# Kernel optimization log

Hardware: AMD Instinct MI355X
Metric: run time of the kernel (lower is better)

## Reference

```python
import jax, jax.numpy as jnp
import numpy as np

H = 128
M = 50000
L = 400000
EPS = 1e-9


def setup_inputs() -> dict:
    key = jax.random.key(0)
    ks = jax.random.split(key, 24)
    d = {
        'x_emb': jax.random.normal(ks[0], (M, H), jnp.float32),
        'child_h': jax.random.normal(ks[1], (M, H), jnp.float32),
        'child_c': jax.random.normal(ks[2], (M, H), jnp.float32),
        'pair_cand_idx': jax.random.randint(ks[3], (L,), 0, M, jnp.int32),
        'pair_child_idx': jax.random.randint(ks[4], (L,), 0, M, jnp.int32),
    }
    s = 1.0 / np.sqrt(H)
    names = ['Wi_w', 'Ui_w', 'Wf_w', 'Uf_w', 'Wo_w', 'Uo_w', 'Wc_w', 'Uc_w', 'Wa_w', 'Ua_w']
    for i, n in enumerate(names):
        d[n] = jax.random.uniform(ks[5 + i], (H, H), jnp.float32, -s, s)
    for i, n in enumerate(['Wi_b', 'Wf_b', 'Wo_b', 'Wc_b', 'Wa_b']):
        d[n] = jax.random.uniform(ks[15 + i], (H,), jnp.float32, -s, s)
    d['v_w'] = jax.random.uniform(ks[20], (H,), jnp.float32, -s, s)
    return d


def reference(x_emb, child_h, child_c, pair_cand_idx, pair_child_idx,
              Wi_w, Ui_w, Wf_w, Uf_w, Wo_w, Uo_w, Wc_w, Uc_w, Wa_w, Ua_w,
              Wi_b, Wf_b, Wo_b, Wc_b, Wa_b, v_w):
    m = x_emb.shape[0]
    ci, chi = pair_cand_idx, pair_child_idx

    # --- segment attention (torch version runs under no_grad) ---
    Ah = child_h @ Wa_w.T + Wa_b          # [M,H]
    Bx = x_emb @ Ua_w.T                   # [M,H]
    e = jnp.tanh(Ah[chi] + Bx[ci]) @ v_w  # [L]
    seg_max = jax.ops.segment_max(e, ci, num_segments=m)
    x_exp = jnp.exp(e - seg_max[ci])
    seg_sum = jax.ops.segment_sum(x_exp, ci, num_segments=m) + EPS
    attn = x_exp / seg_sum[ci]            # [L]
    h_hat = jax.ops.segment_sum(attn[:, None] * child_h[chi], ci, num_segments=m)  # [M,H]

    # --- tree-LSTM gates ---
    i_j = jax.nn.sigmoid(x_emb @ Wi_w.T + Wi_b + h_hat @ Ui_w.T)
    Wfx = x_emb @ Wf_w.T + Wf_b
    Ufh = child_h @ Uf_w.T
    f_pair = jax.nn.sigmoid(Wfx[ci] + Ufh[chi])                       # [L,H]
    sum_f_c = jax.ops.segment_sum(f_pair * child_c[chi], ci, num_segments=m)
    c_t = jnp.tanh(x_emb @ Wc_w.T + Wc_b + h_hat @ Uc_w.T)
    c = i_j * c_t + sum_f_c
    o_j = jax.nn.sigmoid(x_emb @ Wo_w.T + Wo_b + h_hat @ Uo_w.T)
    h = o_j * jnp.tanh(c)
    return (h, c)
```

## Files before the change

kernel.cpp:

```cpp
#include <hip/hip_runtime.h>
#include <cstdint>
#include <cstddef>

#define H 128
#define PSTRIDE 512

typedef __bf16 v8bf __attribute__((ext_vector_type(8)));
typedef __bf16 v4bf __attribute__((ext_vector_type(4)));
typedef float  v4f  __attribute__((ext_vector_type(4)));

__device__ __forceinline__ float ftanh(float x) {
    return 1.f - 2.f / (1.f + __expf(2.f * x));
}
__device__ __forceinline__ float fsigm(float x) {
    return 1.f / (1.f + __expf(-x));
}

struct Stage { const __bf16* W; const float* bias; __bf16* C; int ldc; };
struct MultiDesc { const void* A; int lda; int af32; int ns; Stage st[5]; };
struct MultiBatch { MultiDesc g[2]; };
struct WPtrs { const float* w[10]; };

__global__ __launch_bounds__(256) void prep_k(WPtrs wp, __bf16* __restrict__ Wb,
                                              const float* __restrict__ chh,
                                              const float* __restrict__ chc,
                                              __bf16* __restrict__ P,
                                              const int* __restrict__ ci,
                                              int* __restrict__ counts,
                                              int MH4, int L) {
    int tid = blockIdx.x * 256 + threadIdx.x;
    if (tid < 40960) {
        int mat = tid >> 12;
        int off = (tid & 4095) << 2;
        v4f a = *(const v4f*)(wp.w[mat] + off);
        v4bf b;
#pragma unroll
        for (int k = 0; k < 4; ++k) b[k] = (__bf16)a[k];
        *(v4bf*)(Wb + mat * 16384 + off) = b;
        return;
    }
    int i = tid - 40960;
    if (i < MH4) {
        v4f b = ((const v4f*)chh)[i];
        v4f c = ((const v4f*)chc)[i];
        v4bf bb, cb;
#pragma unroll
        for (int k = 0; k < 4; ++k) { bb[k] = (__bf16)b[k]; cb[k] = (__bf16)c[k]; }
        int m = i >> 5;
        int q = (i & 31) << 2;
        __bf16* prow = P + (size_t)m * PSTRIDE + q;
        *(v4bf*)prow = bb;
        *(v4bf*)(prow + H) = cb;
        return;
    }
    int l = i - MH4;
    if (l < L) atomicAdd(&counts[ci[l]], 1);
}

__global__ __launch_bounds__(256) void gemm_multi(MultiBatch mb, int M) {
    const MultiDesc d = mb.g[blockIdx.y];
    __shared__ __bf16 wlds[H][H + 8];

    const int wave = threadIdx.x >> 6;
    const int lane = threadIdx.x & 63;
    const int quad = lane >> 4;
    const int l16  = lane & 15;
    const int r0   = blockIdx.x * 128 + wave * 32;

    int ra = r0 + l16;      if (ra > M - 1) ra = M - 1;
    int rb = r0 + 16 + l16; if (rb > M - 1) rb = M - 1;

    v8bf a0[4], a1[4];
    if (d.af32) {
        const float* A = (const float*)d.A;
        const float* p0 = A + (size_t)ra * d.lda + quad * 8;
        const float* p1 = A + (size_t)rb * d.lda + quad * 8;
#pragma unroll
        for (int k0 = 0; k0 < 4; ++k0) {
            v4f x0a = *(const v4f*)(p0 + k0 * 32);
            v4f x0b = *(const v4f*)(p0 + k0 * 32 + 4);
            v4f x1a = *(const v4f*)(p1 + k0 * 32);
            v4f x1b = *(const v4f*)(p1 + k0 * 32 + 4);
            v8bf t0, t1;
#pragma unroll
            for (int k = 0; k < 4; ++k) {
                t0[k] = (__bf16)x0a[k]; t0[k + 4] = (__bf16)x0b[k];
                t1[k] = (__bf16)x1a[k]; t1[k + 4] = (__bf16)x1b[k];
            }
            a0[k0] = t0; a1[k0] = t1;
        }
    } else {
        const __bf16* A = (const __bf16*)d.A;
        const __bf16* p0 = A + (size_t)ra * d.lda + quad * 8;
        const __bf16* p1 = A + (size_t)rb * d.lda + quad * 8;
#pragma unroll
        for (int k0 = 0; k0 < 4; ++k0) {
            a0[k0] = *(const v8bf*)(p0 + k0 * 32);
            a1[k0] = *(const v8bf*)(p1 + k0 * 32);
        }
    }

    for (int s = 0; s < d.ns; ++s) {
        if (s) __syncthreads();
        for (int t = threadIdx.x; t < 2048; t += 256) {
            int n = t >> 4;
            int k = (t & 15) << 3;
            *(v8bf*)&wlds[n][k] = *(const v8bf*)(d.st[s].W + n * H + k);
        }
        __syncthreads();

        v4f acc0[8], acc1[8];
#pragma unroll
        for (int nt = 0; nt < 8; ++nt) {
            acc0[nt] = (v4f){0.f, 0.f, 0.f, 0.f};
            acc1[nt] = (v4f){0.f, 0.f, 0.f, 0.f};
        }
#pragma unroll
        for (int k0 = 0; k0 < 4; ++k0) {
#pragma unroll
            for (int nt = 0; nt < 8; ++nt) {
                v8bf b = *(const v8bf*)(&wlds[nt * 16 + l16][k0 * 32 + quad * 8]);
                acc0[nt] = __builtin_amdgcn_mfma_f32_16x16x32_bf16(a0[k0], b, acc0[nt], 0, 0, 0);
                acc1[nt] = __builtin_amdgcn_mfma_f32_16x16x32_bf16(a1[k0], b, acc1[nt], 0, 0, 0);
            }
        }

        const float* bias = d.st[s].bias;
        __bf16* C = d.st[s].C;
        const int ldc = d.st[s].ldc;
#pragma unroll
        for (int nt = 0; nt < 8; ++nt) {
            int n = nt * 16 + l16;
            float bia = bias ? bias[n] : 0.f;
#pragma unroll
            for (int r = 0; r < 4; ++r) {
                int m0 = r0 + quad * 4 + r;
                int m1 = m0 + 16;
                if (m0 < M) C[(size_t)m0 * ldc + n] = (__bf16)(acc0[nt][r] + bia);
                if (m1 < M) C[(size_t)m1 * ldc + n] = (__bf16)(acc1[nt][r] + bia);
            }
        }
    }
}

__global__ __launch_bounds__(256) void edge_score(const int* __restrict__ ci,
                                                  const int* __restrict__ chi,
                                                  const float* __restrict__ vw,
                                                  const __bf16* __restrict__ Bx,
                                                  const __bf16* __restrict__ P,
                                                  float* __restrict__ ex_out, int L) {
    int e = blockIdx.x * 8 + (threadIdx.x >> 5);
    if (e >= L) return;
    const int l32 = threadIdx.x & 31;
    const int h = l32 << 2;
    int m  = ci[e];
    int cj = chi[e];

    v4bf a4 = *(const v4bf*)(P + (cj << 9) + 3 * H + h);
    v4bf b4 = *(const v4bf*)(Bx + (m << 7) + h);
    v4f  vv = *(const v4f*)(vw + h);

    float s = 0.f;
#pragma unroll
    for (int k = 0; k < 4; ++k) s += ftanh((float)a4[k] + (float)b4[k]) * vv[k];
    s += __shfl_xor(s, 1);
    s += __shfl_xor(s, 2);
    s += __shfl_xor(s, 4);
    s += __shfl_xor(s, 8);
    s += __shfl_xor(s, 16);
    if (l32 == 0) ex_out[e] = __expf(s);
}

__global__ __launch_bounds__(1024) void scan_local(const int* __restrict__ counts,
                                                   int* __restrict__ excl,
                                                   int* __restrict__ bsums, int M) {
    __shared__ int s[1024];
    int tid = threadIdx.x;
    int idx = blockIdx.x * 1024 + tid;
    int v = (idx < M) ? counts[idx] : 0;
    s[tid] = v;
    __syncthreads();
    for (int off = 1; off < 1024; off <<= 1) {
        int t = (tid >= off) ? s[tid - off] : 0;
        __syncthreads();
        s[tid] += t;
        __syncthreads();
    }
    if (idx < M) excl[idx] = s[tid] - v;
    if (tid == 1023) bsums[blockIdx.x] = s[1023];
}

__global__ __launch_bounds__(1024) void scan_fused(int* __restrict__ rowptr,
                                                   int* __restrict__ cursor,
                                                   const int* __restrict__ bsums,
                                                   const int* __restrict__ counts,
                                                   int M, int nb) {
    __shared__ int s[1024];
    int t = threadIdx.x, b = blockIdx.x;
    int v = (t < nb) ? bsums[t] : 0;
    s[t] = v;
    __syncthreads();
    for (int off = 1; off < 1024; off <<= 1) {
        int tt = (t >= off) ? s[t - off] : 0;
        __syncthreads();
        s[t] += tt;
        __syncthreads();
    }
    int boff = (b == 0) ? 0 : s[b - 1];
    int idx = b * 1024 + t;
    if (idx < M) {
        int val = rowptr[idx] + boff;
        rowptr[idx] = val;
        cursor[idx] = val;
        if (idx == M - 1) rowptr[M] = val + counts[M - 1];
    }
}

__global__ __launch_bounds__(256) void scatter_k(const int* __restrict__ ci,
                                                 const int* __restrict__ chi,
                                                 const float* __restrict__ ex_e,
                                                 int* __restrict__ cursor,
                                                 int* __restrict__ payload,
                                                 float* __restrict__ exs, int L) {
    int l = blockIdx.x * 256 + threadIdx.x;
    if (l < L) {
        float ex = ex_e[l];
        int c = chi[l];
        int pos = atomicAdd(&cursor[ci[l]], 1);
        payload[pos] = c;
        exs[pos] = ex;
    }
}

__global__ __launch_bounds__(256) void segment_fused(const int* __restrict__ rowptr,
                                                     const int* __restrict__ payload,
                                                     const float* __restrict__ exs,
                                                     const __bf16* __restrict__ Wfx,
                                                     const __bf16* __restrict__ P,
                                                     __bf16* __restrict__ hhat,
                                                     float* __restrict__ sumfc, int M) {
    const int wl   = threadIdx.x & 63;
    const int half = wl & 32;
    const int l32  = wl & 31;
    const int m = blockIdx.x * 8 + (threadIdx.x >> 5);
    if (m >= M) return;
    const int start = rowptr[m];
    const int deg   = rowptr[m + 1] - start;
    const int h = l32 << 2;

    v4bf wf4 = *(const v4bf*)(Wfx + (m << 7) + h);
    float wff[4];
#pragma unroll
    for (int k = 0; k < 4; ++k) wff[k] = (float)wf4[k];

    int   pl0 = (l32 < deg) ? payload[start + l32] : 0;
    int   pl1 = (32 + l32 < deg) ? payload[start + 32 + l32] : 0;
    float ex0 = (l32 < deg) ? exs[start + l32] : 0.f;
    float ex1 = (32 + l32 < deg) ? exs[start + 32 + l32] : 0.f;

    float denom = 0.f;
    float acch[4] = {0.f, 0.f, 0.f, 0.f};
    float accf[4] = {0.f, 0.f, 0.f, 0.f};

    const int jcap = deg < 64 ? deg : 64;
    for (int j = 0; j < jcap; ++j) {
        int   cj = __shfl((j & 32) ? pl1 : pl0, half | (j & 31), 64);
        float ex = __shfl((j & 32) ? ex1 : ex0, half | (j & 31), 64);
        int off = (cj << 9) + h;
        v4bf h4 = *(const v4bf*)(P + off);
        v4bf c4 = *(const v4bf*)(P + off + H);
        v4bf u4 = *(const v4bf*)(P + off + 2 * H);
        denom += ex;
#pragma unroll
        for (int k = 0; k < 4; ++k) {
            acch[k] = fmaf(ex, (float)h4[k], acch[k]);
            accf[k] += fsigm(wff[k] + (float)u4[k]) * (float)c4[k];
        }
    }
    for (int j = 64; j < deg; ++j) {
        int   cj = payload[start + j];
        float ex = exs[start + j];
        int off = (cj << 9) + h;
        v4bf h4 = *(const v4bf*)(P + off);
        v4bf c4 = *(const v4bf*)(P + off + H);
        v4bf u4 = *(const v4bf*)(P + off + 2 * H);
        denom += ex;
#pragma unroll
        for (int k = 0; k < 4; ++k) {
            acch[k] = fmaf(ex, (float)h4[k], acch[k]);
            accf[k] += fsigm(wff[k] + (float)u4[k]) * (float)c4[k];
        }
    }

    float inv = 1.f / (denom + 1e-9f);
    v4bf hb;
    v4f sf;
#pragma unroll
    for (int k = 0; k < 4; ++k) { hb[k] = (__bf16)(acch[k] * inv); sf[k] = accf[k]; }
    *(v4bf*)(hhat + (size_t)m * H + h) = hb;
    *(v4f*)(sumfc + (size_t)m * H + h) = sf;
}

__global__ __launch_bounds__(256) void gemm_final(const __bf16* __restrict__ hhat,
                                                  const __bf16* __restrict__ Ui,
                                                  const __bf16* __restrict__ Uc,
                                                  const __bf16* __restrict__ Uo,
                                                  const __bf16* __restrict__ Xi,
                                                  const __bf16* __restrict__ Xc,
                                                  const __bf16* __restrict__ Xo,
                                                  const float* __restrict__ sumfc,
                                                  float* __restrict__ out, int M, int MH) {
    __shared__ __bf16 wl[3][H][H + 8];

    for (int t = threadIdx.x; t < 6144; t += 256) {
        int w = t >> 11;
        int n = (t >> 4) & 127;
        int k = (t & 15) << 3;
        const __bf16* src = (w == 0) ? Ui : (w == 1) ? Uc : Uo;
        *(v8bf*)&wl[w][n][k] = *(const v8bf*)(src + n * H + k);
    }
    __syncthreads();

    const int wave = threadIdx.x >> 6;
    const int lane = threadIdx.x & 63;
    const int quad = lane >> 4;
    const int l16  = lane & 15;
    const int r0   = blockIdx.x * 128 + wave * 32;

    const __bf16* p0 = hhat + (size_t)(r0 + l16) * H + quad * 8;
    const __bf16* p1 = hhat + (size_t)(r0 + 16 + l16) * H + quad * 8;
    v8bf a0[4], a1[4];
#pragma unroll
    for (int k0 = 0; k0 < 4; ++k0) {
        a0[k0] = *(const v8bf*)(p0 + k0 * 32);
        a1[k0] = *(const v8bf*)(p1 + k0 * 32);
    }

#pragma unroll
    for (int nt = 0; nt < 8; ++nt) {
        v4f ai0 = (v4f){0.f, 0.f, 0.f, 0.f}, ai1 = ai0;
        v4f ac0 = ai0, ac1 = ai0, ao0 = ai0, ao1 = ai0;
#pragma unroll
        for (int k0 = 0; k0 < 4; ++k0) {
            v8bf bi = *(const v8bf*)(&wl[0][nt * 16 + l16][k0 * 32 + quad * 8]);
            v8bf bc = *(const v8bf*)(&wl[1][nt * 16 + l16][k0 * 32 + quad * 8]);
            v8bf bo = *(const v8bf*)(&wl[2][nt * 16 + l16][k0 * 32 + quad * 8]);
            ai0 = __builtin_amdgcn_mfma_f32_16x16x32_bf16(a0[k0], bi, ai0, 0, 0, 0);
            ai1 = __builtin_amdgcn_mfma_f32_16x16x32_bf16(a1[k0], bi, ai1, 0, 0, 0);
            ac0 = __builtin_amdgcn_mfma_f32_16x16x32_bf16(a0[k0], bc, ac0, 0, 0, 0);
            ac1 = __builtin_amdgcn_mfma_f32_16x16x32_bf16(a1[k0], bc, ac1, 0, 0, 0);
            ao0 = __builtin_amdgcn_mfma_f32_16x16x32_bf16(a0[k0], bo, ao0, 0, 0, 0);
            ao1 = __builtin_amdgcn_mfma_f32_16x16x32_bf16(a1[k0], bo, ao1, 0, 0, 0);
        }
        int n = nt * 16 + l16;
#pragma unroll
        for (int r = 0; r < 4; ++r) {
            int m0 = r0 + quad * 4 + r;
            if (m0 < M) {
                size_t idx = (size_t)m0 * H + n;
                float ig = fsigm((float)Xi[idx] + ai0[r]);
                float ct = ftanh((float)Xc[idx] + ac0[r]);
                float og = fsigm((float)Xo[idx] + ao0[r]);
                float c = ig * ct + sumfc[idx];
                out[idx] = og * ftanh(c);
                out[MH + idx] = c;
            }
            int m1 = m0 + 16;
            if (m1 < M) {
                size_t idx = (size_t)m1 * H + n;
                float ig = fsigm((float)Xi[idx] + ai1[r]);
                float ct = ftanh((float)Xc[idx] + ac1[r]);
                float og = fsigm((float)Xo[idx] + ao1[r]);
                float c = ig * ct + sumfc[idx];
                out[idx] = og * ftanh(c);
                out[MH + idx] = c;
            }
        }
    }
}

extern "C" void kernel_launch(void* const* d_in, const int* in_sizes, int n_in,
                              void* d_out, int out_size, void* d_ws, size_t ws_size,
                              hipStream_t stream) {
    const float* x_emb   = (const float*)d_in[0];
    const float* child_h = (const float*)d_in[1];
    const float* child_c = (const float*)d_in[2];
    const int*   ci      = (const int*)d_in[3];
    const int*   chi     = (const int*)d_in[4];
    const float* Wi_b = (const float*)d_in[15];
    const float* Wf_b = (const float*)d_in[16];
    const float* Wo_b = (const float*)d_in[17];
    const float* Wc_b = (const float*)d_in[18];
    const float* Wa_b = (const float*)d_in[19];
    const float* vw   = (const float*)d_in[20];

    const int M    = in_sizes[0] / H;
    const int L    = in_sizes[3];
    const int Mpad = (M + 127) & ~127;
    const int MH   = M * H;
    const int MH4  = MH / 4;

    char* p = (char*)d_ws;
    auto alloc = [&](size_t bytes) {
        char* r = p;
        p += (bytes + 255) & ~(size_t)255;
        return (void*)r;
    };
    size_t bfbytes = (size_t)Mpad * H * sizeof(__bf16);
    __bf16* P      = (__bf16*)alloc((size_t)Mpad * PSTRIDE * sizeof(__bf16));
    __bf16* hhat16 = (__bf16*)alloc(bfbytes);
    __bf16* Bx16   = (__bf16*)alloc(bfbytes);
    __bf16* Wfx16  = (__bf16*)alloc(bfbytes);
    __bf16* Xi16   = (__bf16*)alloc(bfbytes);
    __bf16* Xc16   = (__bf16*)alloc(bfbytes);
    __bf16* Xo16   = (__bf16*)alloc(bfbytes);
    __bf16* Wb     = (__bf16*)alloc(10 * 16384 * sizeof(__bf16));
    float* sumfc   = (float*)alloc((size_t)MH * 4);
    float* ex_e    = (float*)alloc((size_t)L * 4);
    float* exs     = (float*)alloc((size_t)L * 4);
    int*   payload = (int*)alloc((size_t)L * 4);
    int*   counts  = (int*)alloc((size_t)M * 4);
    int*   rowptr  = (int*)alloc((size_t)(M + 1) * 4);
    int*   cursor  = (int*)alloc((size_t)M * 4);
    int*   bsums   = (int*)alloc(1024 * 4);

    hipMemsetAsync(counts, 0, (size_t)M * 4, stream);

    WPtrs wp;
    for (int k = 0; k < 10; ++k) wp.w[k] = (const float*)d_in[5 + k];
    int prep_items = 40960 + MH4 + L;
    prep_k<<<(prep_items + 255) / 256, 256, 0, stream>>>(wp, Wb, child_h, child_c,
                                                         P, ci, counts, MH4, L);

    const __bf16* Wi = Wb + 0 * 16384;
    const __bf16* Ui = Wb + 1 * 16384;
    const __bf16* Wf = Wb + 2 * 16384;
    const __bf16* Uf = Wb + 3 * 16384;
    const __bf16* Wo = Wb + 4 * 16384;
    const __bf16* Uo = Wb + 5 * 16384;
    const __bf16* Wc = Wb + 6 * 16384;
    const __bf16* Uc = Wb + 7 * 16384;
    const __bf16* Wa = Wb + 8 * 16384;
    const __bf16* Ua = Wb + 9 * 16384;

    MultiBatch mb{};
    mb.g[0].A = x_emb; mb.g[0].lda = H; mb.g[0].af32 = 1; mb.g[0].ns = 5;
    mb.g[0].st[0] = Stage{Ua, nullptr, Bx16, H};
    mb.g[0].st[1] = Stage{Wf, Wf_b, Wfx16, H};
    mb.g[0].st[2] = Stage{Wi, Wi_b, Xi16, H};
    mb.g[0].st[3] = Stage{Wc, Wc_b, Xc16, H};
    mb.g[0].st[4] = Stage{Wo, Wo_b, Xo16, H};
    mb.g[1].A = P; mb.g[1].lda = PSTRIDE; mb.g[1].af32 = 0; mb.g[1].ns = 2;
    mb.g[1].st[0] = Stage{Wa, Wa_b, P + 3 * H, PSTRIDE};
    mb.g[1].st[1] = Stage{Uf, nullptr, P + 2 * H, PSTRIDE};
    gemm_multi<<<dim3(Mpad / 128, 2), 256, 0, stream>>>(mb, M);

    edge_score<<<(L + 7) / 8, 256, 0, stream>>>(ci, chi, vw, Bx16, P, ex_e, L);

    int nb = (M + 1023) / 1024;
    scan_local<<<nb, 1024, 0, stream>>>(counts, rowptr, bsums, M);
    scan_fused<<<nb, 1024, 0, stream>>>(rowptr, cursor, bsums, counts, M, nb);

    scatter_k<<<(L + 255) / 256, 256, 0, stream>>>(ci, chi, ex_e, cursor, payload, exs, L);

    segment_fused<<<(M + 7) / 8, 256, 0, stream>>>(rowptr, payload, exs, Wfx16, P,
                                                   hhat16, sumfc, M);

    gemm_final<<<Mpad / 128, 256, 0, stream>>>(hhat16, Ui, Uc, Uo, Xi16, Xc16, Xo16,
                                               sumfc, (float*)d_out, M, MH);
}
```

Before: 479.5 us.

## Split multi-stage GEMM into one block per weight, pre-convert x_emb to bf16

```diff
diff --git a/kernel.cpp b/kernel.cpp
--- a/kernel.cpp
+++ b/kernel.cpp
@@ -16,14 +16,22 @@
     return 1.f / (1.f + __expf(-x));
 }
 
-struct Stage { const __bf16* W; const float* bias; __bf16* C; int ldc; };
-struct MultiDesc { const void* A; int lda; int af32; int ns; Stage st[5]; };
-struct MultiBatch { MultiDesc g[2]; };
+struct MatDesc {
+    const __bf16* A;
+    int           lda;
+    const __bf16* Wb;
+    const float*  bias;
+    __bf16*       C;
+    int           ldc;
+};
+struct MatBatch { MatDesc m[7]; };
 struct WPtrs { const float* w[10]; };
 
 __global__ __launch_bounds__(256) void prep_k(WPtrs wp, __bf16* __restrict__ Wb,
+                                              const float* __restrict__ x,
                                               const float* __restrict__ chh,
                                               const float* __restrict__ chc,
+                                              __bf16* __restrict__ xe,
                                               __bf16* __restrict__ P,
                                               const int* __restrict__ ci,
                                               int* __restrict__ counts,
@@ -41,11 +49,15 @@
     }
     int i = tid - 40960;
     if (i < MH4) {
+        v4f a = ((const v4f*)x)[i];
         v4f b = ((const v4f*)chh)[i];
         v4f c = ((const v4f*)chc)[i];
-        v4bf bb, cb;
-#pragma unroll
-        for (int k = 0; k < 4; ++k) { bb[k] = (__bf16)b[k]; cb[k] = (__bf16)c[k]; }
+        v4bf ab, bb, cb;
+#pragma unroll
+        for (int k = 0; k < 4; ++k) {
+            ab[k] = (__bf16)a[k]; bb[k] = (__bf16)b[k]; cb[k] = (__bf16)c[k];
+        }
+        ((v4bf*)xe)[i] = ab;
         int m = i >> 5;
         int q = (i & 31) << 2;
         __bf16* prow = P + (size_t)m * PSTRIDE + q;
@@ -57,9 +69,16 @@
     if (l < L) atomicAdd(&counts[ci[l]], 1);
 }
 
-__global__ __launch_bounds__(256) void gemm_multi(MultiBatch mb, int M) {
-    const MultiDesc d = mb.g[blockIdx.y];
+__global__ __launch_bounds__(256) void gemm_batch(MatBatch batch, int M) {
+    const MatDesc d = batch.m[blockIdx.y];
     __shared__ __bf16 wlds[H][H + 8];
+
+    for (int t = threadIdx.x; t < 2048; t += 256) {
+        int n = t >> 4;
+        int k = (t & 15) << 3;
+        *(v8bf*)&wlds[n][k] = *(const v8bf*)(d.Wb + n * H + k);
+    }
+    __syncthreads();
 
     const int wave = threadIdx.x >> 6;
     const int lane = threadIdx.x & 63;
@@ -67,78 +86,37 @@
     const int l16  = lane & 15;
     const int r0   = blockIdx.x * 128 + wave * 32;
 
-    int ra = r0 + l16;      if (ra > M - 1) ra = M - 1;
-    int rb = r0 + 16 + l16; if (rb > M - 1) rb = M - 1;
-
-    v8bf a0[4], a1[4];
-    if (d.af32) {
-        const float* A = (const float*)d.A;
-        const float* p0 = A + (size_t)ra * d.lda + quad * 8;
-        const float* p1 = A + (size_t)rb * d.lda + quad * 8;
-#pragma unroll
-        for (int k0 = 0; k0 < 4; ++k0) {
-            v4f x0a = *(const v4f*)(p0 + k0 * 32);
-            v4f x0b = *(const v4f*)(p0 + k0 * 32 + 4);
-            v4f x1a = *(const v4f*)(p1 + k0 * 32);
-            v4f x1b = *(const v4f*)(p1 + k0 * 32 + 4);
-            v8bf t0, t1;
-#pragma unroll
-            for (int k = 0; k < 4; ++k) {
-                t0[k] = (__bf16)x0a[k]; t0[k + 4] = (__bf16)x0b[k];
-                t1[k] = (__bf16)x1a[k]; t1[k + 4] = (__bf16)x1b[k];
-            }
-            a0[k0] = t0; a1[k0] = t1;
-        }
-    } else {
-        const __bf16* A = (const __bf16*)d.A;
-        const __bf16* p0 = A + (size_t)ra * d.lda + quad * 8;
-        const __bf16* p1 = A + (size_t)rb * d.lda + quad * 8;
-#pragma unroll
-        for (int k0 = 0; k0 < 4; ++k0) {
-            a0[k0] = *(const v8bf*)(p0 + k0 * 32);
-            a1[k0] = *(const v8bf*)(p1 + k0 * 32);
-        }
-    }
-
-    for (int s = 0; s < d.ns; ++s) {
-        if (s) __syncthreads();
-        for (int t = threadIdx.x; t < 2048; t += 256) {
-            int n = t >> 4;
-            int k = (t & 15) << 3;
-            *(v8bf*)&wlds[n][k] = *(const v8bf*)(d.st[s].W + n * H + k);
-        }
-        __syncthreads();
-
-        v4f acc0[8], acc1[8];
+    v4f acc0[8], acc1[8];
+#pragma unroll
+    for (int nt = 0; nt < 8; ++nt) {
+        acc0[nt] = (v4f){0.f, 0.f, 0.f, 0.f};
+        acc1[nt] = (v4f){0.f, 0.f, 0.f, 0.f};
+    }
+
+    const __bf16* ar0 = d.A + (size_t)(r0 + l16) * d.lda + quad * 8;
+    const __bf16* ar1 = d.A + (size_t)(r0 + 16 + l16) * d.lda + quad * 8;
+#pragma unroll
+    for (int k0 = 0; k0 < H; k0 += 32) {
+        v8bf a0 = *(const v8bf*)(ar0 + k0);
+        v8bf a1 = *(const v8bf*)(ar1 + k0);
 #pragma unroll
         for (int nt = 0; nt < 8; ++nt) {
-            acc0[nt] = (v4f){0.f, 0.f, 0.f, 0.f};
-            acc1[nt] = (v4f){0.f, 0.f, 0.f, 0.f};
-        }
-#pragma unroll
-        for (int k0 = 0; k0 < 4; ++k0) {
-#pragma unroll
-            for (int nt = 0; nt < 8; ++nt) {
-                v8bf b = *(const v8bf*)(&wlds[nt * 16 + l16][k0 * 32 + quad * 8]);
-                acc0[nt] = __builtin_amdgcn_mfma_f32_16x16x32_bf16(a0[k0], b, acc0[nt], 0, 0, 0);
-                acc1[nt] = __builtin_amdgcn_mfma_f32_16x16x32_bf16(a1[k0], b, acc1[nt], 0, 0, 0);
-            }
-        }
-
-        const float* bias = d.st[s].bias;
-        __bf16* C = d.st[s].C;
-        const int ldc = d.st[s].ldc;
-#pragma unroll
-        for (int nt = 0; nt < 8; ++nt) {
-            int n = nt * 16 + l16;
-            float bia = bias ? bias[n] : 0.f;
-#pragma unroll
-            for (int r = 0; r < 4; ++r) {
-                int m0 = r0 + quad * 4 + r;
-                int m1 = m0 + 16;
-                if (m0 < M) C[(size_t)m0 * ldc + n] = (__bf16)(acc0[nt][r] + bia);
-                if (m1 < M) C[(size_t)m1 * ldc + n] = (__bf16)(acc1[nt][r] + bia);
-            }
+            v8bf b = *(const v8bf*)(&wlds[nt * 16 + l16][k0 + quad * 8]);
+            acc0[nt] = __builtin_amdgcn_mfma_f32_16x16x32_bf16(a0, b, acc0[nt], 0, 0, 0);
+            acc1[nt] = __builtin_amdgcn_mfma_f32_16x16x32_bf16(a1, b, acc1[nt], 0, 0, 0);
+        }
+    }
+
+#pragma unroll
+    for (int nt = 0; nt < 8; ++nt) {
+        int n = nt * 16 + l16;
+        float bia = d.bias ? d.bias[n] : 0.f;
+#pragma unroll
+        for (int r = 0; r < 4; ++r) {
+            int m0 = r0 + quad * 4 + r;
+            int m1 = m0 + 16;
+            if (m0 < M) d.C[(size_t)m0 * d.ldc + n] = (__bf16)(acc0[nt][r] + bia);
+            if (m1 < M) d.C[(size_t)m1 * d.ldc + n] = (__bf16)(acc1[nt][r] + bia);
         }
     }
 }
@@ -301,7 +279,7 @@
     *(v4f*)(sumfc + (size_t)m * H + h) = sf;
 }
 
-__global__ __launch_bounds__(256) void gemm_final(const __bf16* __restrict__ hhat,
+__global__ __launch_bounds__(512) void gemm_final(const __bf16* __restrict__ hhat,
                                                   const __bf16* __restrict__ Ui,
                                                   const __bf16* __restrict__ Uc,
                                                   const __bf16* __restrict__ Uo,
@@ -312,7 +290,7 @@
                                                   float* __restrict__ out, int M, int MH) {
     __shared__ __bf16 wl[3][H][H + 8];
 
-    for (int t = threadIdx.x; t < 6144; t += 256) {
+    for (int t = threadIdx.x; t < 6144; t += 512) {
         int w = t >> 11;
         int n = (t >> 4) & 127;
         int k = (t & 15) << 3;
@@ -325,32 +303,25 @@
     const int lane = threadIdx.x & 63;
     const int quad = lane >> 4;
     const int l16  = lane & 15;
-    const int r0   = blockIdx.x * 128 + wave * 32;
+    const int r0   = blockIdx.x * 128 + wave * 16;
 
     const __bf16* p0 = hhat + (size_t)(r0 + l16) * H + quad * 8;
-    const __bf16* p1 = hhat + (size_t)(r0 + 16 + l16) * H + quad * 8;
-    v8bf a0[4], a1[4];
-#pragma unroll
-    for (int k0 = 0; k0 < 4; ++k0) {
-        a0[k0] = *(const v8bf*)(p0 + k0 * 32);
-        a1[k0] = *(const v8bf*)(p1 + k0 * 32);
-    }
+    v8bf a0[4];
+#pragma unroll
+    for (int k0 = 0; k0 < 4; ++k0) a0[k0] = *(const v8bf*)(p0 + k0 * 32);
 
 #pragma unroll
     for (int nt = 0; nt < 8; ++nt) {
-        v4f ai0 = (v4f){0.f, 0.f, 0.f, 0.f}, ai1 = ai0;
-        v4f ac0 = ai0, ac1 = ai0, ao0 = ai0, ao1 = ai0;
+        v4f ai0 = (v4f){0.f, 0.f, 0.f, 0.f};
+        v4f ac0 = ai0, ao0 = ai0;
 #pragma unroll
         for (int k0 = 0; k0 < 4; ++k0) {
             v8bf bi = *(const v8bf*)(&wl[0][nt * 16 + l16][k0 * 32 + quad * 8]);
             v8bf bc = *(const v8bf*)(&wl[1][nt * 16 + l16][k0 * 32 + quad * 8]);
             v8bf bo = *(const v8bf*)(&wl[2][nt * 16 + l16][k0 * 32 + quad * 8]);
             ai0 = __builtin_amdgcn_mfma_f32_16x16x32_bf16(a0[k0], bi, ai0, 0, 0, 0);
-            ai1 = __builtin_amdgcn_mfma_f32_16x16x32_bf16(a1[k0], bi, ai1, 0, 0, 0);
             ac0 = __builtin_amdgcn_mfma_f32_16x16x32_bf16(a0[k0], bc, ac0, 0, 0, 0);
-            ac1 = __builtin_amdgcn_mfma_f32_16x16x32_bf16(a1[k0], bc, ac1, 0, 0, 0);
             ao0 = __builtin_amdgcn_mfma_f32_16x16x32_bf16(a0[k0], bo, ao0, 0, 0, 0);
-            ao1 = __builtin_amdgcn_mfma_f32_16x16x32_bf16(a1[k0], bo, ao1, 0, 0, 0);
         }
         int n = nt * 16 + l16;
 #pragma unroll
@@ -361,16 +332,6 @@
                 float ig = fsigm((float)Xi[idx] + ai0[r]);
                 float ct = ftanh((float)Xc[idx] + ac0[r]);
                 float og = fsigm((float)Xo[idx] + ao0[r]);
-                float c = ig * ct + sumfc[idx];
-                out[idx] = og * ftanh(c);
-                out[MH + idx] = c;
-            }
-            int m1 = m0 + 16;
-            if (m1 < M) {
-                size_t idx = (size_t)m1 * H + n;
-                float ig = fsigm((float)Xi[idx] + ai1[r]);
-                float ct = ftanh((float)Xc[idx] + ac1[r]);
-                float og = fsigm((float)Xo[idx] + ao1[r]);
                 float c = ig * ct + sumfc[idx];
                 out[idx] = og * ftanh(c);
                 out[MH + idx] = c;
@@ -407,6 +368,7 @@
         return (void*)r;
     };
     size_t bfbytes = (size_t)Mpad * H * sizeof(__bf16);
+    __bf16* xe16   = (__bf16*)alloc(bfbytes);
     __bf16* P      = (__bf16*)alloc((size_t)Mpad * PSTRIDE * sizeof(__bf16));
     __bf16* hhat16 = (__bf16*)alloc(bfbytes);
     __bf16* Bx16   = (__bf16*)alloc(bfbytes);
@@ -429,8 +391,8 @@
     WPtrs wp;
     for (int k = 0; k < 10; ++k) wp.w[k] = (const float*)d_in[5 + k];
     int prep_items = 40960 + MH4 + L;
-    prep_k<<<(prep_items + 255) / 256, 256, 0, stream>>>(wp, Wb, child_h, child_c,
-                                                         P, ci, counts, MH4, L);
+    prep_k<<<(prep_items + 255) / 256, 256, 0, stream>>>(wp, Wb, x_emb, child_h, child_c,
+                                                         xe16, P, ci, counts, MH4, L);
 
     const __bf16* Wi = Wb + 0 * 16384;
     const __bf16* Ui = Wb + 1 * 16384;
@@ -443,17 +405,16 @@
     const __bf16* Wa = Wb + 8 * 16384;
     const __bf16* Ua = Wb + 9 * 16384;
 
-    MultiBatch mb{};
-    mb.g[0].A = x_emb; mb.g[0].lda = H; mb.g[0].af32 = 1; mb.g[0].ns = 5;
-    mb.g[0].st[0] = Stage{Ua, nullptr, Bx16, H};
-    mb.g[0].st[1] = Stage{Wf, Wf_b, Wfx16, H};
-    mb.g[0].st[2] = Stage{Wi, Wi_b, Xi16, H};
-    mb.g[0].st[3] = Stage{Wc, Wc_b, Xc16, H};
-    mb.g[0].st[4] = Stage{Wo, Wo_b, Xo16, H};
-    mb.g[1].A = P; mb.g[1].lda = PSTRIDE; mb.g[1].af32 = 0; mb.g[1].ns = 2;
-    mb.g[1].st[0] = Stage{Wa, Wa_b, P + 3 * H, PSTRIDE};
-    mb.g[1].st[1] = Stage{Uf, nullptr, P + 2 * H, PSTRIDE};
-    gemm_multi<<<dim3(Mpad / 128, 2), 256, 0, stream>>>(mb, M);
+    MatBatch ba{};
+    ba.m[0] = MatDesc{P,    PSTRIDE, Wa, Wa_b,    P + 3 * H, PSTRIDE};
+    ba.m[1] = MatDesc{xe16, H,       Ua, nullptr, Bx16,      H};
+    ba.m[2] = MatDesc{xe16, H,       Wf, Wf_b,    Wfx16,     H};
+    ba.m[3] = MatDesc{P,    PSTRIDE, Uf, nullptr, P + 2 * H, PSTRIDE};
+    ba.m[4] = MatDesc{xe16, H,       Wi, Wi_b,    Xi16,      H};
+    ba.m[5] = MatDesc{xe16, H,       Wc, Wc_b,    Xc16,      H};
+    ba.m[6] = MatDesc{xe16, H,       Wo, Wo_b,    Xo16,      H};
+    dim3 gA(Mpad / 128, 7);
+    gemm_batch<<<gA, 256, 0, stream>>>(ba, M);
 
     edge_score<<<(L + 7) / 8, 256, 0, stream>>>(ci, chi, vw, Bx16, P, ex_e, L);
 
@@ -466,6 +427,6 @@
     segment_fused<<<(M + 7) / 8, 256, 0, stream>>>(rowptr, payload, exs, Wfx16, P,
                                                    hhat16, sumfc, M);
 
-    gemm_final<<<Mpad / 128, 256, 0, stream>>>(hhat16, Ui, Uc, Uo, Xi16, Xc16, Xo16,
+    gemm_final<<<Mpad / 128, 512, 0, stream>>>(hhat16, Ui, Uc, Uo, Xi16, Xc16, Xo16,
                                                sumfc, (float*)d_out, M, MH);
 }
```

Measured after the change: 417.8 us. -12.9%, faster.
